# Kernel tuning notes

Measured on AMD Instinct MI355X. Metric: run time of the kernel, lower is better.

## Reference

```python
import jax, jax.numpy as jnp
import numpy as np

N = 50000   # nodes per type (d and t)
E = 500000  # edges per relation
D = 128     # in = out features
NEG_SLOPE = 0.2


def setup_inputs() -> dict:
    key = jax.random.key(0)
    ks = jax.random.split(key, 24)
    s = 1.0 / np.sqrt(D)
    inp = {
        'x_d': jax.random.normal(ks[0], (N, D), jnp.float32),
        'x_t': jax.random.normal(ks[1], (N, D), jnp.float32),
        'W_dd': jax.random.normal(ks[2], (D, D), jnp.float32) * s,
        'W_tt': jax.random.normal(ks[3], (D, D), jnp.float32) * s,
        'W_dt': jax.random.normal(ks[4], (D, D), jnp.float32) * s,
        'al_dd': jax.random.normal(ks[5], (D,), jnp.float32) * s,
        'ar_dd': jax.random.normal(ks[6], (D,), jnp.float32) * s,
        'al_tt': jax.random.normal(ks[7], (D,), jnp.float32) * s,
        'ar_tt': jax.random.normal(ks[8], (D,), jnp.float32) * s,
        'al_dt': jax.random.normal(ks[9], (D,), jnp.float32) * s,
        'ar_dt': jax.random.normal(ks[10], (D,), jnp.float32) * s,
        'b_dd': jnp.zeros((D,), jnp.float32),
        'b_tt': jnp.zeros((D,), jnp.float32),
        'b_dt': jnp.zeros((D,), jnp.float32),
        'src_dd': jax.random.randint(ks[11], (E,), 0, N),
        'dst_dd': jax.random.randint(ks[12], (E,), 0, N),
        'src_tt': jax.random.randint(ks[13], (E,), 0, N),
        'dst_tt': jax.random.randint(ks[14], (E,), 0, N),
        'src_dt': jax.random.randint(ks[15], (E,), 0, N),
        'dst_dt': jax.random.randint(ks[16], (E,), 0, N),
        'src_td': jax.random.randint(ks[17], (E,), 0, N),
        'dst_td': jax.random.randint(ks[18], (E,), 0, N),
    }
    return inp


def _gat(x_src, x_dst, W, al, ar, b, src, dst, n_dst):
    """DGL GATConv (num_heads=1, no dropout, eval): gather -> edge attn ->
    per-destination segment softmax -> scatter-weighted aggregation + bias."""
    fs = x_src @ W                      # [Ns, D]
    fd = x_dst @ W                      # [Nd, D]
    el = fs @ al                        # [Ns]
    er = fd @ ar                        # [Nd]
    e = jax.nn.leaky_relu(el[src] + er[dst], NEG_SLOPE)   # [E]
    m = jax.ops.segment_max(e, dst, num_segments=n_dst)
    m = jnp.where(jnp.isfinite(m), m, jnp.float32(0))      # isolated dst nodes
    ex = jnp.exp(e - m[dst])
    ssum = jax.ops.segment_sum(ex, dst, num_segments=n_dst)
    alpha = ex / ssum[dst]              # [E]
    out = jax.ops.segment_sum(alpha[:, None] * fs[src], dst, num_segments=n_dst)
    return out + b


def reference(x_d, x_t, W_dd, W_tt, W_dt,
              al_dd, ar_dd, al_tt, ar_tt, al_dt, ar_dt,
              b_dd, b_tt, b_dt,
              src_dd, dst_dd, src_tt, dst_tt,
              src_dt, dst_dt, src_td, dst_td):
    # HeteroGraphConv with aggregate='sum'; 'dt' and 'td' share parameters.
    h_d = (_gat(x_d, x_d, W_dd, al_dd, ar_dd, b_dd, src_dd, dst_dd, N)
           + _gat(x_t, x_d, W_dt, al_dt, ar_dt, b_dt, src_td, dst_td, N))
    h_t = (_gat(x_t, x_t, W_tt, al_tt, ar_tt, b_tt, src_tt, dst_tt, N)
           + _gat(x_d, x_t, W_dt, al_dt, ar_dt, b_dt, src_dt, dst_dt, N))
    return jnp.stack([h_d, h_t])        # [2, N, D]
```

## Files before the change

kernel.cpp:

```cpp
#include <hip/hip_runtime.h>
#include <hip/hip_bf16.h>
#include <hip/hip_fp16.h>
#include <math.h>

#define DD 128
#define NEG_SLOPE 0.2f
#define CAP_B 2048
#define BSHIFT 7
#define MAXNB 512
#define NSCAT 160

typedef __attribute__((ext_vector_type(8))) short bf16x8;
typedef __attribute__((ext_vector_type(4))) float f32x4;
typedef __attribute__((ext_vector_type(8))) unsigned short u16x8;

__device__ __forceinline__ short f2bf(float f) {
    __hip_bfloat16 h = __float2bfloat16(f);
    return __builtin_bit_cast(short, h);
}
__device__ __forceinline__ float bf2f(unsigned short u) {
    return __uint_as_float(((unsigned)u) << 16);
}
__device__ __forceinline__ unsigned short f2h(float f) {
    return __builtin_bit_cast(unsigned short, __float2half(f));
}
__device__ __forceinline__ float h2f(unsigned short u) {
    return __half2float(__builtin_bit_cast(__half, u));
}
__device__ __forceinline__ float lrexp(float e) {
    e = (e > 0.f) ? e : NEG_SLOPE * e;
    return __expf(e);
}

__device__ __forceinline__ int permcol(int cp) { return (cp & 7) * 16 + (cp >> 3); }

__global__ __launch_bounds__(256) void pack_init_k(
    const float* __restrict__ W0, const float* __restrict__ W1,
    const float* __restrict__ W2,
    unsigned short* __restrict__ P0, unsigned short* __restrict__ P1,
    unsigned short* __restrict__ P2, int* __restrict__ cursor,
    const float* __restrict__ b_dd, const float* __restrict__ b_tt,
    const float* __restrict__ b_dt, float* __restrict__ pb0,
    float* __restrict__ pb1)
{
    if (blockIdx.x >= 24) {
        const int i = (blockIdx.x - 24) * 256 + threadIdx.x;
        if (i < 4 * MAXNB) cursor[i] = (i & (MAXNB - 1)) * CAP_B;
        if (blockIdx.x == 24) {
            const int t = threadIdx.x;
            if (t < 128) pb0[t] = b_dd[permcol(t)] + b_dt[permcol(t)];
            else         pb1[t - 128] = b_tt[permcol(t - 128)] + b_dt[permcol(t - 128)];
        }
        return;
    }
    const int t = blockIdx.x * 256 + threadIdx.x;
    const int m = t >> 11;
    const int r = t & 2047;
    const float* W = (m == 0) ? W0 : (m == 1) ? W1 : W2;
    unsigned short* P = (m == 0) ? P0 : (m == 1) ? P1 : P2;
    const int lane = r & 63;
    const int tile = r >> 6;
    const int ks = tile >> 3, ct = tile & 7;
    const int col = ct * 16 + (lane & 15);
    const int k0 = ks * 32 + (lane >> 4) * 8;
#pragma unroll
    for (int j = 0; j < 8; ++j)
        P[(size_t)r * 8 + j] = (unsigned short)f2bf(W[(size_t)(k0 + j) * DD + col]);
}

__device__ __forceinline__ void epi_store(
    f32x4 acc[8], const float* __restrict__ al, const float* __restrict__ ar,
    unsigned short* __restrict__ fb, float* __restrict__ el,
    float* __restrict__ er, int r0, int lane, int nrows)
{
    float pl[4] = {0.f, 0.f, 0.f, 0.f};
    float pr[4] = {0.f, 0.f, 0.f, 0.f};
#pragma unroll
    for (int ct = 0; ct < 8; ++ct) {
        const float alc = al[ct * 16 + (lane & 15)];
        const float arc = ar[ct * 16 + (lane & 15)];
#pragma unroll
        for (int g = 0; g < 4; ++g) {
            pl[g] = fmaf(acc[ct][g], alc, pl[g]);
            pr[g] = fmaf(acc[ct][g], arc, pr[g]);
        }
    }
#pragma unroll
    for (int o = 1; o < 16; o <<= 1) {
#pragma unroll
        for (int g = 0; g < 4; ++g) {
            pl[g] += __shfl_xor(pl[g], o, 16);
            pr[g] += __shfl_xor(pr[g], o, 16);
        }
    }
    if ((lane & 15) == 0) {
#pragma unroll
        for (int g = 0; g < 4; ++g) {
            const int r = r0 + (lane >> 4) * 4 + g;
            if (r < nrows) { el[r] = pl[g]; er[r] = pr[g]; }
        }
    }
#pragma unroll
    for (int g = 0; g < 4; ++g) {
        const int r = r0 + (lane >> 4) * 4 + g;
        if (r < nrows) {
            u16x8 v;
#pragma unroll
            for (int ct = 0; ct < 8; ++ct)
                v[ct] = (unsigned short)f2bf(acc[ct][g]);
            *((u16x8*)(fb + (size_t)r * DD + (lane & 15) * 8)) = v;
        }
    }
}

struct Prep5Args {
    const float* x[4];
    const unsigned short* Wp[4];
    const float* al[4]; const float* ar[4];
    unsigned short* fb[4]; float* el[4]; float* er[4];
    const int* src[4]; const int* dst[4];
    int* cursor; unsigned* ebuf;
    int n, nE, nb;
};

__global__ __launch_bounds__(512) void prep5_k(Prep5Args P)
{
    __shared__ unsigned short wlds[2048 * 8];

    const int v = blockIdx.y;
    if (v < 4) {
        const int lane = threadIdx.x & 63;
        const int wave = threadIdx.x >> 6;
        const int r0 = (blockIdx.x * 8 + wave) * 16;
        if (blockIdx.x * 128 >= P.n) return;

        const uint4* wsrc = (const uint4*)P.Wp[v];
        uint4* wdst = (uint4*)wlds;
#pragma unroll
        for (int i = 0; i < 4; ++i)
            wdst[threadIdx.x + i * 512] = wsrc[threadIdx.x + i * 512];
        __syncthreads();

        if (r0 >= P.n) return;
        const int arow = r0 + (lane & 15);
        const int arow_c = (arow < P.n) ? arow : (P.n - 1);
        const int kbase = (lane >> 4) * 8;
        const float* x = P.x[v];

        f32x4 acc[8];
#pragma unroll
        for (int ct = 0; ct < 8; ++ct) acc[ct] = (f32x4)(0.f);

#pragma unroll
        for (int ks = 0; ks < 4; ++ks) {
            const float* xp = x + (size_t)arow_c * DD + ks * 32 + kbase;
            const float4 a0 = ((const float4*)xp)[0];
            const float4 a1 = ((const float4*)xp)[1];
            bf16x8 af;
            af[0] = f2bf(a0.x); af[1] = f2bf(a0.y); af[2] = f2bf(a0.z); af[3] = f2bf(a0.w);
            af[4] = f2bf(a1.x); af[5] = f2bf(a1.y); af[6] = f2bf(a1.z); af[7] = f2bf(a1.w);
#pragma unroll
            for (int ct = 0; ct < 8; ++ct) {
                const bf16x8 w = *((const bf16x8*)(wlds + ((size_t)(ks * 8 + ct) * 64 + lane) * 8));
                acc[ct] = __builtin_amdgcn_mfma_f32_16x16x32_bf16(af, w, acc[ct], 0, 0, 0);
            }
        }
        epi_store(acc, P.al[v], P.ar[v], P.fb[v], P.el[v], P.er[v], r0, lane, P.n);
        return;
    }

    const int sb = blockIdx.x;
    if (sb >= 4 * NSCAT) return;
    int* cnt_s  = (int*)wlds;
    int* base_s = ((int*)wlds) + MAXNB;
    const int rel = sb / NSCAT;
    const int blk = sb - rel * NSCAT;
    const int* src = P.src[rel];
    const int* dst = P.dst[rel];
    int* cur = P.cursor + (size_t)rel * MAXNB;
    unsigned* eb = P.ebuf + (size_t)rel * P.nb * CAP_B;

    const int t = threadIdx.x;
    const int ch = (P.nE + NSCAT - 1) / NSCAT;
    const int i0 = blk * ch;
    const int i1 = (i0 + ch < P.nE) ? (i0 + ch) : P.nE;

    for (int i = t; i < MAXNB; i += 512) cnt_s[i] = 0;
    __syncthreads();
    for (int i = i0 + t; i < i1; i += 512)
        atomicAdd(&cnt_s[dst[i] >> BSHIFT], 1);
    __syncthreads();
    for (int b = t; b < P.nb; b += 512) {
        const int c = cnt_s[b];
        base_s[b] = c ? atomicAdd(cur + b, c) : 0;
        cnt_s[b] = 0;
    }
    __syncthreads();
    for (int i = i0 + t; i < i1; i += 512) {
        const int dv = dst[i];
        const int b = dv >> BSHIFT;
        const int p = base_s[b] + atomicAdd(&cnt_s[b], 1);
        eb[p] = ((unsigned)(dv & ((1 << BSHIFT) - 1)) << 16) | (unsigned)src[i];
    }
}

struct SortArgs {
    const float* el[4]; const float* er[4];
};

__global__ __launch_bounds__(256) void sort_alpha_k(
    const unsigned* __restrict__ ebuf, const int* __restrict__ cursor,
    SortArgs S, unsigned* __restrict__ cs32, int* __restrict__ rstart,
    int* __restrict__ rdeg, int n, int nb)
{
    const int b = blockIdx.x, rel = blockIdx.y, t = threadIdx.x;
    int cnt = cursor[(size_t)rel * MAXNB + b] - b * CAP_B;
    cnt = (cnt < 0) ? 0 : (cnt > CAP_B) ? CAP_B : cnt;

    __shared__ unsigned buf[CAP_B];
    __shared__ unsigned out32[CAP_B];
    __shared__ int hist[128], off[128], cnt2[128], excl[128];
    __shared__ float ssum[128];
    __shared__ int total_s;

    const unsigned* ebr = ebuf + ((size_t)rel * nb + b) * CAP_B;
    for (int i = t; i < cnt; i += 256) buf[i] = ebr[i];
    if (t < 128) { hist[t] = 0; cnt2[t] = 0; ssum[t] = 0.f; }
    __syncthreads();
    for (int i = t; i < cnt; i += 256) atomicAdd(&hist[buf[i] >> 16], 1);
    __syncthreads();
    if (t < 128) off[t] = (hist[t] + 3) & ~3;
    __syncthreads();
    for (int o = 1; o < 128; o <<= 1) {
        const int v = (t < 128 && t >= o) ? off[t - o] : 0;
        __syncthreads();
        if (t < 128) off[t] += v;
        __syncthreads();
    }
    if (t < 128) {
        const int pc = (hist[t] + 3) & ~3;
        excl[t] = off[t] - pc;
        const int d = b * 128 + t;
        if (d < n) {
            rstart[(size_t)rel * n + d] = b * CAP_B + excl[t];
            rdeg[(size_t)rel * n + d] = pc;
        }
        for (int i = excl[t] + hist[t]; i < off[t]; ++i) out32[i] = 0u;
    }
    if (t == 127) total_s = off[127];
    __syncthreads();

    const float* el = S.el[rel];
    const float* er = S.er[rel];
    for (int i = t; i < cnt; i += 256) {
        const unsigned v = buf[i];
        const int local = v >> 16;
        const int s = v & 0xffffu;
        const float ex = lrexp(el[s] + er[b * 128 + local]);
        atomicAdd(&ssum[local], ex);
        const int p = excl[local] + atomicAdd(&cnt2[local], 1);
        out32[p] = (unsigned)s | ((unsigned)f2h(ex) << 16);
    }
    __syncthreads();
    if (t < 128 && hist[t] > 0) {
        const float inv = 1.f / ssum[t];
        const int e0 = excl[t], e1 = excl[t] + hist[t];
        for (int i = e0; i < e1; ++i) {
            const unsigned v = out32[i];
            const float alpha = h2f((unsigned short)(v >> 16)) * inv;
            out32[i] = (v & 0xffffu) | ((unsigned)f2h(alpha) << 16);
        }
    }
    __syncthreads();
    unsigned* cs = cs32 + ((size_t)rel * nb + b) * CAP_B;
    const int total = total_s;
    for (int i = t; i < total; i += 256) cs[i] = out32[i];
}

struct AggArgs {
    const int* rs[4]; const int* rd[4];
    const unsigned* cs[4];
    const unsigned short* fb[4];
    const float* pb[2];
    float* out[2];
    int n;
};

__device__ __forceinline__ void fma8(
    float a, const u16x8& v, float4& o0, float4& o1)
{
    o0.x = fmaf(a, bf2f(v[0]), o0.x);
    o0.y = fmaf(a, bf2f(v[1]), o0.y);
    o0.z = fmaf(a, bf2f(v[2]), o0.z);
    o0.w = fmaf(a, bf2f(v[3]), o0.w);
    o1.x = fmaf(a, bf2f(v[4]), o1.x);
    o1.y = fmaf(a, bf2f(v[5]), o1.y);
    o1.z = fmaf(a, bf2f(v[6]), o1.z);
    o1.w = fmaf(a, bf2f(v[7]), o1.w);
}

__device__ __forceinline__ void agg16p(
    const int* __restrict__ rs, const int* __restrict__ rd,
    const unsigned* __restrict__ cs, const unsigned short* __restrict__ fb,
    int d, int lane, float4& o0, float4& o1)
{
    const int cnt = rd[d];
    if (cnt == 0) return;
    const unsigned* csp = cs + rs[d];
    int k = 0;
    for (; k + 8 <= cnt; k += 8) {
        unsigned pv[8];
#pragma unroll
        for (int j = 0; j < 8; ++j) pv[j] = csp[k + j];
        u16x8 v[8];
#pragma unroll
        for (int j = 0; j < 8; ++j)
            v[j] = ((const u16x8*)(fb + (size_t)(pv[j] & 0xffffu) * DD))[lane];
#pragma unroll
        for (int j = 0; j < 8; ++j)
            fma8(h2f((unsigned short)(pv[j] >> 16)), v[j], o0, o1);
    }
    for (; k + 4 <= cnt; k += 4) {
        unsigned pv[4];
#pragma unroll
        for (int j = 0; j < 4; ++j) pv[j] = csp[k + j];
        u16x8 v[4];
#pragma unroll
        for (int j = 0; j < 4; ++j)
            v[j] = ((const u16x8*)(fb + (size_t)(pv[j] & 0xffffu) * DD))[lane];
#pragma unroll
        for (int j = 0; j < 4; ++j)
            fma8(h2f((unsigned short)(pv[j] >> 16)), v[j], o0, o1);
    }
}

__global__ __launch_bounds__(256) void gat_aggregate_f(AggArgs A)
{
    const int lane = threadIdx.x & 15;
    const int grp  = threadIdx.x >> 4;
    const int gid = blockIdx.x * 16 + grp;
    if (gid >= 2 * A.n) return;
    const int ty = (gid >= A.n) ? 1 : 0;
    const int d = gid - ty * A.n;
    const int sl1 = ty ? 1 : 0;
    const int sl2 = ty ? 2 : 3;

    float4 o0 = ((const float4*)A.pb[ty])[lane * 2];
    float4 o1 = ((const float4*)A.pb[ty])[lane * 2 + 1];

    agg16p(A.rs[sl1], A.rd[sl1], A.cs[sl1], A.fb[sl1], d, lane, o0, o1);
    agg16p(A.rs[sl2], A.rd[sl2], A.cs[sl2], A.fb[sl2], d, lane, o0, o1);

    float* op = A.out[ty] + (size_t)d * DD + lane;
    op[0]   = o0.x; op[16]  = o0.y; op[32]  = o0.z; op[48]  = o0.w;
    op[64]  = o1.x; op[80]  = o1.y; op[96]  = o1.z; op[112] = o1.w;
}

extern "C" void kernel_launch(void* const* d_in, const int* in_sizes, int n_in,
                              void* d_out, int out_size, void* d_ws, size_t ws_size,
                              hipStream_t stream)
{
    const float* x_d  = (const float*)d_in[0];
    const float* x_t  = (const float*)d_in[1];
    const float* W_dd = (const float*)d_in[2];
    const float* W_tt = (const float*)d_in[3];
    const float* W_dt = (const float*)d_in[4];
    const float* al_dd = (const float*)d_in[5];
    const float* ar_dd = (const float*)d_in[6];
    const float* al_tt = (const float*)d_in[7];
    const float* ar_tt = (const float*)d_in[8];
    const float* al_dt = (const float*)d_in[9];
    const float* ar_dt = (const float*)d_in[10];
    const float* b_dd  = (const float*)d_in[11];
    const float* b_tt  = (const float*)d_in[12];
    const float* b_dt  = (const float*)d_in[13];
    const int* src_dd = (const int*)d_in[14];
    const int* dst_dd = (const int*)d_in[15];
    const int* src_tt = (const int*)d_in[16];
    const int* dst_tt = (const int*)d_in[17];
    const int* src_dt = (const int*)d_in[18];
    const int* dst_dt = (const int*)d_in[19];
    const int* src_td = (const int*)d_in[20];
    const int* dst_td = (const int*)d_in[21];

    const int n  = in_sizes[0] / DD;
    const int nE = in_sizes[14];
    const int nb = (n + 127) >> BSHIFT;

    float* ws = (float*)d_ws;
    size_t off = 0;
    unsigned short* fb_dd   = (unsigned short*)(ws + off); off += (size_t)n * DD / 2;
    unsigned short* fb_tt   = (unsigned short*)(ws + off); off += (size_t)n * DD / 2;
    unsigned short* fb_dt_d = (unsigned short*)(ws + off); off += (size_t)n * DD / 2;
    unsigned short* fb_dt_t = (unsigned short*)(ws + off); off += (size_t)n * DD / 2;
    unsigned* ebuf = (unsigned*)(ws + off); off += (size_t)4 * nb * CAP_B;
    unsigned* cs32 = (unsigned*)(ws + off); off += (size_t)4 * nb * CAP_B;
    float* el_dd   = ws + off; off += n;
    float* er_dd   = ws + off; off += n;
    float* el_tt   = ws + off; off += n;
    float* er_tt   = ws + off; off += n;
    float* el_dt_d = ws + off; off += n;
    float* er_dt_d = ws + off; off += n;
    float* el_dt_t = ws + off; off += n;
    float* er_dt_t = ws + off; off += n;
    int* rstart = (int*)(ws + off); off += (size_t)4 * n;
    int* rdeg   = (int*)(ws + off); off += (size_t)4 * n;
    int* cursor = (int*)(ws + off); off += (size_t)4 * MAXNB;
    unsigned short* Wp_dd = (unsigned short*)(ws + off); off += 2048 * 8 / 2;
    unsigned short* Wp_tt = (unsigned short*)(ws + off); off += 2048 * 8 / 2;
    unsigned short* Wp_dt = (unsigned short*)(ws + off); off += 2048 * 8 / 2;
    float* pb0 = ws + off; off += DD;
    float* pb1 = ws + off; off += DD;

    if (ws_size < off * sizeof(float)) return;

    pack_init_k<<<32, 256, 0, stream>>>(W_dd, W_tt, W_dt, Wp_dd, Wp_tt, Wp_dt,
                                        cursor, b_dd, b_tt, b_dt, pb0, pb1);

    Prep5Args P;
    P.x[0] = x_d; P.x[1] = x_t; P.x[2] = x_d; P.x[3] = x_t;
    P.Wp[0] = Wp_dd; P.Wp[1] = Wp_tt; P.Wp[2] = Wp_dt; P.Wp[3] = Wp_dt;
    P.al[0] = al_dd; P.al[1] = al_tt; P.al[2] = al_dt; P.al[3] = al_dt;
    P.ar[0] = ar_dd; P.ar[1] = ar_tt; P.ar[2] = ar_dt; P.ar[3] = ar_dt;
    P.fb[0] = fb_dd; P.fb[1] = fb_tt; P.fb[2] = fb_dt_d; P.fb[3] = fb_dt_t;
    P.el[0] = el_dd; P.el[1] = el_tt; P.el[2] = el_dt_d; P.el[3] = el_dt_t;
    P.er[0] = er_dd; P.er[1] = er_tt; P.er[2] = er_dt_d; P.er[3] = er_dt_t;
    P.src[0] = src_dd; P.dst[0] = dst_dd;
    P.src[1] = src_tt; P.dst[1] = dst_tt;
    P.src[2] = src_dt; P.dst[2] = dst_dt;
    P.src[3] = src_td; P.dst[3] = dst_td;
    P.cursor = cursor; P.ebuf = ebuf;
    P.n = n; P.nE = nE; P.nb = nb;

    int gx = (n + 127) / 128;
    if (gx < 4 * NSCAT) gx = 4 * NSCAT;
    dim3 pgrid(gx, 5);
    prep5_k<<<pgrid, 512, 0, stream>>>(P);

    SortArgs S;
    S.el[0] = el_dd;   S.er[0] = er_dd;
    S.el[1] = el_tt;   S.er[1] = er_tt;
    S.el[2] = el_dt_d; S.er[2] = er_dt_t;
    S.el[3] = el_dt_t; S.er[3] = er_dt_d;
    dim3 bgrid(nb, 4);
    sort_alpha_k<<<bgrid, 256, 0, stream>>>(ebuf, cursor, S, cs32, rstart, rdeg, n, nb);

    const size_t reg = (size_t)nb * CAP_B;
    AggArgs A;
    A.rs[0] = rstart + 0 * (size_t)n; A.rd[0] = rdeg + 0 * (size_t)n;
    A.rs[1] = rstart + 1 * (size_t)n; A.rd[1] = rdeg + 1 * (size_t)n;
    A.rs[2] = rstart + 2 * (size_t)n; A.rd[2] = rdeg + 2 * (size_t)n;
    A.rs[3] = rstart + 3 * (size_t)n; A.rd[3] = rdeg + 3 * (size_t)n;
    A.cs[0] = cs32 + 0 * reg; A.cs[1] = cs32 + 1 * reg;
    A.cs[2] = cs32 + 2 * reg; A.cs[3] = cs32 + 3 * reg;
    A.fb[0] = fb_dd; A.fb[1] = fb_tt;
    A.fb[2] = fb_dt_d;
    A.fb[3] = fb_dt_t;
    A.pb[0] = pb0; A.pb[1] = pb1;
    A.out[0] = (float*)d_out;
    A.out[1] = (float*)d_out + (size_t)n * DD;
    A.n = n;

    const int aggrid = (2 * n + 15) / 16;
    gat_aggregate_f<<<aggrid, 256, 0, stream>>>(A);
}
```

Baseline: 145.1 us.

## Use persistent tiled GEMM blocks and per-block multi-relation scatter in prep kernel

The prep kernel now launches a fixed grid of 160 blocks per relation. Each GEMM block loads the packed weight into LDS once and loops over row tiles with a stride, instead of one block per 128-row tile that reloads W every time. The scatter blocks each handle their edge chunk for all four relations in sequence, instead of one block per relation-chunk. This cuts the block count and redundant weight loads, but lowers parallelism for the scatter phase and adds serial work per block.

```diff
diff --git a/kernel.cpp b/kernel.cpp
--- a/kernel.cpp
+++ b/kernel.cpp
@@ -9,6 +9,7 @@
 #define BSHIFT 7
 #define MAXNB 512
 #define NSCAT 160
+#define TBLK 160
 
 typedef __attribute__((ext_vector_type(8))) short bf16x8;
 typedef __attribute__((ext_vector_type(4))) float f32x4;
@@ -113,94 +114,96 @@
     }
 }
 
-struct Prep5Args {
+struct Prep6Args {
     const float* x[4];
     const unsigned short* Wp[4];
     const float* al[4]; const float* ar[4];
     unsigned short* fb[4]; float* el[4]; float* er[4];
     const int* src[4]; const int* dst[4];
     int* cursor; unsigned* ebuf;
-    int n, nE, nb;
+    int n, nE, nb, ntiles;
 };
 
-__global__ __launch_bounds__(512) void prep5_k(Prep5Args P)
+__global__ __launch_bounds__(512) void prep6_k(Prep6Args P)
 {
     __shared__ unsigned short wlds[2048 * 8];
 
     const int v = blockIdx.y;
     if (v < 4) {
+        const uint4* wsrc = (const uint4*)P.Wp[v];
+        uint4* wdst = (uint4*)wlds;
+#pragma unroll
+        for (int i = 0; i < 4; ++i)
+            wdst[threadIdx.x + i * 512] = wsrc[threadIdx.x + i * 512];
+        __syncthreads();
+
         const int lane = threadIdx.x & 63;
         const int wave = threadIdx.x >> 6;
-        const int r0 = (blockIdx.x * 8 + wave) * 16;
-        if (blockIdx.x * 128 >= P.n) return;
-
-        const uint4* wsrc = (const uint4*)P.Wp[v];
-        uint4* wdst = (uint4*)wlds;
-#pragma unroll
-        for (int i = 0; i < 4; ++i)
-            wdst[threadIdx.x + i * 512] = wsrc[threadIdx.x + i * 512];
-        __syncthreads();
-
-        if (r0 >= P.n) return;
-        const int arow = r0 + (lane & 15);
-        const int arow_c = (arow < P.n) ? arow : (P.n - 1);
         const int kbase = (lane >> 4) * 8;
         const float* x = P.x[v];
 
-        f32x4 acc[8];
-#pragma unroll
-        for (int ct = 0; ct < 8; ++ct) acc[ct] = (f32x4)(0.f);
-
-#pragma unroll
-        for (int ks = 0; ks < 4; ++ks) {
-            const float* xp = x + (size_t)arow_c * DD + ks * 32 + kbase;
-            const float4 a0 = ((const float4*)xp)[0];
-            const float4 a1 = ((const float4*)xp)[1];
-            bf16x8 af;
-            af[0] = f2bf(a0.x); af[1] = f2bf(a0.y); af[2] = f2bf(a0.z); af[3] = f2bf(a0.w);
-            af[4] = f2bf(a1.x); af[5] = f2bf(a1.y); af[6] = f2bf(a1.z); af[7] = f2bf(a1.w);
-#pragma unroll
-            for (int ct = 0; ct < 8; ++ct) {
-                const bf16x8 w = *((const bf16x8*)(wlds + ((size_t)(ks * 8 + ct) * 64 + lane) * 8));
-                acc[ct] = __builtin_amdgcn_mfma_f32_16x16x32_bf16(af, w, acc[ct], 0, 0, 0);
+        for (int tile = blockIdx.x; tile < P.ntiles; tile += TBLK) {
+            const int r0 = (tile * 8 + wave) * 16;
+            if (r0 >= P.n) continue;
+            const int arow = r0 + (lane & 15);
+            const int arow_c = (arow < P.n) ? arow : (P.n - 1);
+
+            f32x4 acc[8];
+#pragma unroll
+            for (int ct = 0; ct < 8; ++ct) acc[ct] = (f32x4)(0.f);
+
+#pragma unroll
+            for (int ks = 0; ks < 4; ++ks) {
+                const float* xp = x + (size_t)arow_c * DD + ks * 32 + kbase;
+                const float4 a0 = ((const float4*)xp)[0];
+                const float4 a1 = ((const float4*)xp)[1];
+                bf16x8 af;
+                af[0] = f2bf(a0.x); af[1] = f2bf(a0.y); af[2] = f2bf(a0.z); af[3] = f2bf(a0.w);
+                af[4] = f2bf(a1.x); af[5] = f2bf(a1.y); af[6] = f2bf(a1.z); af[7] = f2bf(a1.w);
+#pragma unroll
+                for (int ct = 0; ct < 8; ++ct) {
+                    const bf16x8 w = *((const bf16x8*)(wlds + ((size_t)(ks * 8 + ct) * 64 + lane) * 8));
+                    acc[ct] = __builtin_amdgcn_mfma_f32_16x16x32_bf16(af, w, acc[ct], 0, 0, 0);
+                }
             }
-        }
-        epi_store(acc, P.al[v], P.ar[v], P.fb[v], P.el[v], P.er[v], r0, lane, P.n);
+            epi_store(acc, P.al[v], P.ar[v], P.fb[v], P.el[v], P.er[v], r0, lane, P.n);
+        }
         return;
     }
 
     const int sb = blockIdx.x;
-    if (sb >= 4 * NSCAT) return;
+    if (sb >= NSCAT) return;
     int* cnt_s  = (int*)wlds;
     int* base_s = ((int*)wlds) + MAXNB;
-    const int rel = sb / NSCAT;
-    const int blk = sb - rel * NSCAT;
-    const int* src = P.src[rel];
-    const int* dst = P.dst[rel];
-    int* cur = P.cursor + (size_t)rel * MAXNB;
-    unsigned* eb = P.ebuf + (size_t)rel * P.nb * CAP_B;
-
     const int t = threadIdx.x;
     const int ch = (P.nE + NSCAT - 1) / NSCAT;
-    const int i0 = blk * ch;
+    const int i0 = sb * ch;
     const int i1 = (i0 + ch < P.nE) ? (i0 + ch) : P.nE;
 
-    for (int i = t; i < MAXNB; i += 512) cnt_s[i] = 0;
-    __syncthreads();
-    for (int i = i0 + t; i < i1; i += 512)
-        atomicAdd(&cnt_s[dst[i] >> BSHIFT], 1);
-    __syncthreads();
-    for (int b = t; b < P.nb; b += 512) {
-        const int c = cnt_s[b];
-        base_s[b] = c ? atomicAdd(cur + b, c) : 0;
-        cnt_s[b] = 0;
-    }
-    __syncthreads();
-    for (int i = i0 + t; i < i1; i += 512) {
-        const int dv = dst[i];
-        const int b = dv >> BSHIFT;
-        const int p = base_s[b] + atomicAdd(&cnt_s[b], 1);
-        eb[p] = ((unsigned)(dv & ((1 << BSHIFT) - 1)) << 16) | (unsigned)src[i];
+    for (int rel = 0; rel < 4; ++rel) {
+        const int* src = P.src[rel];
+        const int* dst = P.dst[rel];
+        int* cur = P.cursor + (size_t)rel * MAXNB;
+        unsigned* eb = P.ebuf + (size_t)rel * P.nb * CAP_B;
+
+        for (int i = t; i < MAXNB; i += 512) cnt_s[i] = 0;
+        __syncthreads();
+        for (int i = i0 + t; i < i1; i += 512)
+            atomicAdd(&cnt_s[dst[i] >> BSHIFT], 1);
+        __syncthreads();
+        for (int b = t; b < P.nb; b += 512) {
+            const int c = cnt_s[b];
+            base_s[b] = c ? atomicAdd(cur + b, c) : 0;
+            cnt_s[b] = 0;
+        }
+        __syncthreads();
+        for (int i = i0 + t; i < i1; i += 512) {
+            const int dv = dst[i];
+            const int b = dv >> BSHIFT;
+            const int p = base_s[b] + atomicAdd(&cnt_s[b], 1);
+            eb[p] = ((unsigned)(dv & ((1 << BSHIFT) - 1)) << 16) | (unsigned)src[i];
+        }
+        __syncthreads();
     }
 }
 
@@ -286,7 +289,7 @@
     int n;
 };
 
-__device__ __forceinline__ void fma8(
+__device__ __forceinline__ void fma8v(
     float a, const u16x8& v, float4& o0, float4& o1)
 {
     o0.x = fmaf(a, bf2f(v[0]), o0.x);
@@ -318,7 +321,7 @@
             v[j] = ((const u16x8*)(fb + (size_t)(pv[j] & 0xffffu) * DD))[lane];
 #pragma unroll
         for (int j = 0; j < 8; ++j)
-            fma8(h2f((unsigned short)(pv[j] >> 16)), v[j], o0, o1);
+            fma8v(h2f((unsigned short)(pv[j] >> 16)), v[j], o0, o1);
     }
     for (; k + 4 <= cnt; k += 4) {
         unsigned pv[4];
@@ -330,7 +333,7 @@
             v[j] = ((const u16x8*)(fb + (size_t)(pv[j] & 0xffffu) * DD))[lane];
 #pragma unroll
         for (int j = 0; j < 4; ++j)
-            fma8(h2f((unsigned short)(pv[j] >> 16)), v[j], o0, o1);
+            fma8v(h2f((unsigned short)(pv[j] >> 16)), v[j], o0, o1);
     }
 }
 
@@ -386,6 +389,7 @@
     const int n  = in_sizes[0] / DD;
     const int nE = in_sizes[14];
     const int nb = (n + 127) >> BSHIFT;
+    const int ntiles = (n + 127) / 128;
 
     float* ws = (float*)d_ws;
     size_t off = 0;
@@ -417,7 +421,7 @@
     pack_init_k<<<32, 256, 0, stream>>>(W_dd, W_tt, W_dt, Wp_dd, Wp_tt, Wp_dt,
                                         cursor, b_dd, b_tt, b_dt, pb0, pb1);
 
-    Prep5Args P;
+    Prep6Args P;
     P.x[0] = x_d; P.x[1] = x_t; P.x[2] = x_d; P.x[3] = x_t;
     P.Wp[0] = Wp_dd; P.Wp[1] = Wp_tt; P.Wp[2] = Wp_dt; P.Wp[3] = Wp_dt;
     P.al[0] = al_dd; P.al[1] = al_tt; P.al[2] = al_dt; P.al[3] = al_dt;
@@ -430,12 +434,10 @@
     P.src[2] = src_dt; P.dst[2] = dst_dt;
     P.src[3] = src_td; P.dst[3] = dst_td;
     P.cursor = cursor; P.ebuf = ebuf;
-    P.n = n; P.nE = nE; P.nb = nb;
-
-    int gx = (n + 127) / 128;
-    if (gx < 4 * NSCAT) gx = 4 * NSCAT;
-    dim3 pgrid(gx, 5);
-    prep5_k<<<pgrid, 512, 0, stream>>>(P);
+    P.n = n; P.nE = nE; P.nb = nb; P.ntiles = ntiles;
+
+    dim3 pgrid(TBLK, 5);
+    prep6_k<<<pgrid, 512, 0, stream>>>(P);
 
     SortArgs S;
     S.el[0] = el_dd;   S.er[0] = er_dd;
```

New measurement: 154.6 us. 6.5% more time.

## Merge both relations per destination type into one CSR with flag bit

Applied to the files above, without the earlier changes.

The sort kernel now handles both relations that feed a destination type in one block. It builds a single combined per-destination edge list in which the high bit marks which relation and feature table each edge uses, and keeps separate softmax sums per relation. The aggregate kernel then walks one list per destination instead of two, which cuts per-node padding to multiples of four and halves the loop overheads and rstart/rdeg loads. In exchange, each block uses twice the shared memory, which may reduce occupancy, only half as many sort blocks are launched, and the gather adds a per-edge select between feature tables.

```diff
diff --git a/kernel.cpp b/kernel.cpp
--- a/kernel.cpp
+++ b/kernel.cpp
@@ -204,30 +204,38 @@
     }
 }
 
-struct SortArgs {
-    const float* el[4]; const float* er[4];
+struct Sort2Args {
+    const float* elA[2]; const float* erA[2];
+    const float* elB[2]; const float* erB[2];
 };
 
-__global__ __launch_bounds__(256) void sort_alpha_k(
+__global__ __launch_bounds__(256) void sort_alpha2_k(
     const unsigned* __restrict__ ebuf, const int* __restrict__ cursor,
-    SortArgs S, unsigned* __restrict__ cs32, int* __restrict__ rstart,
+    Sort2Args S, unsigned* __restrict__ cs32, int* __restrict__ rstart,
     int* __restrict__ rdeg, int n, int nb)
 {
-    const int b = blockIdx.x, rel = blockIdx.y, t = threadIdx.x;
-    int cnt = cursor[(size_t)rel * MAXNB + b] - b * CAP_B;
-    cnt = (cnt < 0) ? 0 : (cnt > CAP_B) ? CAP_B : cnt;
-
-    __shared__ unsigned buf[CAP_B];
-    __shared__ unsigned out32[CAP_B];
+    const int b = blockIdx.x, ty = blockIdx.y, t = threadIdx.x;
+    const int relA = ty;
+    const int relB = ty ? 2 : 3;
+    int cntA = cursor[(size_t)relA * MAXNB + b] - b * CAP_B;
+    cntA = (cntA < 0) ? 0 : (cntA > CAP_B) ? CAP_B : cntA;
+    int cntB = cursor[(size_t)relB * MAXNB + b] - b * CAP_B;
+    cntB = (cntB < 0) ? 0 : (cntB > CAP_B) ? CAP_B : cntB;
+    const int cnt = cntA + cntB;
+
+    __shared__ unsigned buf[2 * CAP_B];
+    __shared__ unsigned out32[2 * CAP_B];
     __shared__ int hist[128], off[128], cnt2[128], excl[128];
-    __shared__ float ssum[128];
+    __shared__ float ssumA[128], ssumB[128];
     __shared__ int total_s;
 
-    const unsigned* ebr = ebuf + ((size_t)rel * nb + b) * CAP_B;
-    for (int i = t; i < cnt; i += 256) buf[i] = ebr[i];
-    if (t < 128) { hist[t] = 0; cnt2[t] = 0; ssum[t] = 0.f; }
-    __syncthreads();
-    for (int i = t; i < cnt; i += 256) atomicAdd(&hist[buf[i] >> 16], 1);
+    const unsigned* ebA = ebuf + ((size_t)relA * nb + b) * CAP_B;
+    const unsigned* ebB = ebuf + ((size_t)relB * nb + b) * CAP_B;
+    for (int i = t; i < cntA; i += 256) buf[i] = ebA[i];
+    for (int i = t; i < cntB; i += 256) buf[cntA + i] = ebB[i] | 0x80000000u;
+    if (t < 128) { hist[t] = 0; cnt2[t] = 0; ssumA[t] = 0.f; ssumB[t] = 0.f; }
+    __syncthreads();
+    for (int i = t; i < cnt; i += 256) atomicAdd(&hist[(buf[i] >> 16) & 0x7f], 1);
     __syncthreads();
     if (t < 128) off[t] = (hist[t] + 3) & ~3;
     __syncthreads();
@@ -242,51 +250,58 @@
         excl[t] = off[t] - pc;
         const int d = b * 128 + t;
         if (d < n) {
-            rstart[(size_t)rel * n + d] = b * CAP_B + excl[t];
-            rdeg[(size_t)rel * n + d] = pc;
+            rstart[(size_t)ty * n + d] = b * (2 * CAP_B) + excl[t];
+            rdeg[(size_t)ty * n + d] = pc;
         }
         for (int i = excl[t] + hist[t]; i < off[t]; ++i) out32[i] = 0u;
     }
     if (t == 127) total_s = off[127];
     __syncthreads();
 
-    const float* el = S.el[rel];
-    const float* er = S.er[rel];
+    const float* elA = S.elA[ty]; const float* erA = S.erA[ty];
+    const float* elB = S.elB[ty]; const float* erB = S.erB[ty];
     for (int i = t; i < cnt; i += 256) {
         const unsigned v = buf[i];
-        const int local = v >> 16;
+        const unsigned flag = v >> 31;
+        const int local = (v >> 16) & 0x7f;
         const int s = v & 0xffffu;
-        const float ex = lrexp(el[s] + er[b * 128 + local]);
-        atomicAdd(&ssum[local], ex);
+        const int d = b * 128 + local;
+        const float e = flag ? (elB[s] + erB[d]) : (elA[s] + erA[d]);
+        const float ex = lrexp(e);
+        atomicAdd(flag ? &ssumB[local] : &ssumA[local], ex);
         const int p = excl[local] + atomicAdd(&cnt2[local], 1);
-        out32[p] = (unsigned)s | ((unsigned)f2h(ex) << 16);
+        out32[p] = (unsigned)s | ((unsigned)f2h(ex) << 16) | (flag << 31);
     }
     __syncthreads();
     if (t < 128 && hist[t] > 0) {
-        const float inv = 1.f / ssum[t];
+        const float invA = (ssumA[t] > 0.f) ? 1.f / ssumA[t] : 0.f;
+        const float invB = (ssumB[t] > 0.f) ? 1.f / ssumB[t] : 0.f;
         const int e0 = excl[t], e1 = excl[t] + hist[t];
         for (int i = e0; i < e1; ++i) {
             const unsigned v = out32[i];
-            const float alpha = h2f((unsigned short)(v >> 16)) * inv;
-            out32[i] = (v & 0xffffu) | ((unsigned)f2h(alpha) << 16);
-        }
-    }
-    __syncthreads();
-    unsigned* cs = cs32 + ((size_t)rel * nb + b) * CAP_B;
+            const unsigned flag = v >> 31;
+            const float a = h2f((unsigned short)((v >> 16) & 0x7fff)) *
+                            (flag ? invB : invA);
+            out32[i] = (v & 0xffffu) | ((unsigned)f2h(a) << 16) | (flag << 31);
+        }
+    }
+    __syncthreads();
+    unsigned* cs = cs32 + ((size_t)ty * nb + b) * (2 * CAP_B);
     const int total = total_s;
     for (int i = t; i < total; i += 256) cs[i] = out32[i];
 }
 
 struct AggArgs {
-    const int* rs[4]; const int* rd[4];
-    const unsigned* cs[4];
-    const unsigned short* fb[4];
+    const int* rs; const int* rd;
+    const unsigned* cs[2];
+    const unsigned short* fbA[2];
+    const unsigned short* fbB[2];
     const float* pb[2];
     float* out[2];
     int n;
 };
 
-__device__ __forceinline__ void fma8(
+__device__ __forceinline__ void fma8v(
     float a, const u16x8& v, float4& o0, float4& o1)
 {
     o0.x = fmaf(a, bf2f(v[0]), o0.x);
@@ -299,41 +314,6 @@
     o1.w = fmaf(a, bf2f(v[7]), o1.w);
 }
 
-__device__ __forceinline__ void agg16p(
-    const int* __restrict__ rs, const int* __restrict__ rd,
-    const unsigned* __restrict__ cs, const unsigned short* __restrict__ fb,
-    int d, int lane, float4& o0, float4& o1)
-{
-    const int cnt = rd[d];
-    if (cnt == 0) return;
-    const unsigned* csp = cs + rs[d];
-    int k = 0;
-    for (; k + 8 <= cnt; k += 8) {
-        unsigned pv[8];
-#pragma unroll
-        for (int j = 0; j < 8; ++j) pv[j] = csp[k + j];
-        u16x8 v[8];
-#pragma unroll
-        for (int j = 0; j < 8; ++j)
-            v[j] = ((const u16x8*)(fb + (size_t)(pv[j] & 0xffffu) * DD))[lane];
-#pragma unroll
-        for (int j = 0; j < 8; ++j)
-            fma8(h2f((unsigned short)(pv[j] >> 16)), v[j], o0, o1);
-    }
-    for (; k + 4 <= cnt; k += 4) {
-        unsigned pv[4];
-#pragma unroll
-        for (int j = 0; j < 4; ++j) pv[j] = csp[k + j];
-        u16x8 v[4];
-#pragma unroll
-        for (int j = 0; j < 4; ++j)
-            v[j] = ((const u16x8*)(fb + (size_t)(pv[j] & 0xffffu) * DD))[lane];
-#pragma unroll
-        for (int j = 0; j < 4; ++j)
-            fma8(h2f((unsigned short)(pv[j] >> 16)), v[j], o0, o1);
-    }
-}
-
 __global__ __launch_bounds__(256) void gat_aggregate_f(AggArgs A)
 {
     const int lane = threadIdx.x & 15;
@@ -342,14 +322,45 @@
     if (gid >= 2 * A.n) return;
     const int ty = (gid >= A.n) ? 1 : 0;
     const int d = gid - ty * A.n;
-    const int sl1 = ty ? 1 : 0;
-    const int sl2 = ty ? 2 : 3;
 
     float4 o0 = ((const float4*)A.pb[ty])[lane * 2];
     float4 o1 = ((const float4*)A.pb[ty])[lane * 2 + 1];
 
-    agg16p(A.rs[sl1], A.rd[sl1], A.cs[sl1], A.fb[sl1], d, lane, o0, o1);
-    agg16p(A.rs[sl2], A.rd[sl2], A.cs[sl2], A.fb[sl2], d, lane, o0, o1);
+    const unsigned short* fbA = A.fbA[ty];
+    const unsigned short* fbB = A.fbB[ty];
+    const int cnt = A.rd[(size_t)ty * A.n + d];
+    if (cnt > 0) {
+        const unsigned* csp = A.cs[ty] + A.rs[(size_t)ty * A.n + d];
+        int k = 0;
+        for (; k + 8 <= cnt; k += 8) {
+            unsigned pv[8];
+#pragma unroll
+            for (int j = 0; j < 8; ++j) pv[j] = csp[k + j];
+            u16x8 v[8];
+#pragma unroll
+            for (int j = 0; j < 8; ++j) {
+                const unsigned short* fb = (pv[j] >> 31) ? fbB : fbA;
+                v[j] = ((const u16x8*)(fb + (size_t)(pv[j] & 0xffffu) * DD))[lane];
+            }
+#pragma unroll
+            for (int j = 0; j < 8; ++j)
+                fma8v(h2f((unsigned short)((pv[j] >> 16) & 0x7fff)), v[j], o0, o1);
+        }
+        for (; k + 4 <= cnt; k += 4) {
+            unsigned pv[4];
+#pragma unroll
+            for (int j = 0; j < 4; ++j) pv[j] = csp[k + j];
+            u16x8 v[4];
+#pragma unroll
+            for (int j = 0; j < 4; ++j) {
+                const unsigned short* fb = (pv[j] >> 31) ? fbB : fbA;
+                v[j] = ((const u16x8*)(fb + (size_t)(pv[j] & 0xffffu) * DD))[lane];
+            }
+#pragma unroll
+            for (int j = 0; j < 4; ++j)
+                fma8v(h2f((unsigned short)((pv[j] >> 16) & 0x7fff)), v[j], o0, o1);
+        }
+    }
 
     float* op = A.out[ty] + (size_t)d * DD + lane;
     op[0]   = o0.x; op[16]  = o0.y; op[32]  = o0.z; op[48]  = o0.w;
@@ -394,7 +405,7 @@
     unsigned short* fb_dt_d = (unsigned short*)(ws + off); off += (size_t)n * DD / 2;
     unsigned short* fb_dt_t = (unsigned short*)(ws + off); off += (size_t)n * DD / 2;
     unsigned* ebuf = (unsigned*)(ws + off); off += (size_t)4 * nb * CAP_B;
-    unsigned* cs32 = (unsigned*)(ws + off); off += (size_t)4 * nb * CAP_B;
+    unsigned* cs32 = (unsigned*)(ws + off); off += (size_t)2 * nb * (2 * CAP_B);
     float* el_dd   = ws + off; off += n;
     float* er_dd   = ws + off; off += n;
     float* el_tt   = ws + off; off += n;
@@ -403,8 +414,8 @@
     float* er_dt_d = ws + off; off += n;
     float* el_dt_t = ws + off; off += n;
     float* er_dt_t = ws + off; off += n;
-    int* rstart = (int*)(ws + off); off += (size_t)4 * n;
-    int* rdeg   = (int*)(ws + off); off += (size_t)4 * n;
+    int* rstart = (int*)(ws + off); off += (size_t)2 * n;
+    int* rdeg   = (int*)(ws + off); off += (size_t)2 * n;
     int* cursor = (int*)(ws + off); off += (size_t)4 * MAXNB;
     unsigned short* Wp_dd = (unsigned short*)(ws + off); off += 2048 * 8 / 2;
     unsigned short* Wp_tt = (unsigned short*)(ws + off); off += 2048 * 8 / 2;
@@ -437,25 +448,20 @@
     dim3 pgrid(gx, 5);
     prep5_k<<<pgrid, 512, 0, stream>>>(P);
 
-    SortArgs S;
-    S.el[0] = el_dd;   S.er[0] = er_dd;
-    S.el[1] = el_tt;   S.er[1] = er_tt;
-    S.el[2] = el_dt_d; S.er[2] = er_dt_t;
-    S.el[3] = el_dt_t; S.er[3] = er_dt_d;
-    dim3 bgrid(nb, 4);
-    sort_alpha_k<<<bgrid, 256, 0, stream>>>(ebuf, cursor, S, cs32, rstart, rdeg, n, nb);
-
-    const size_t reg = (size_t)nb * CAP_B;
+    Sort2Args S;
+    S.elA[0] = el_dd;   S.erA[0] = er_dd;
+    S.elA[1] = el_tt;   S.erA[1] = er_tt;
+    S.elB[0] = el_dt_t; S.erB[0] = er_dt_d;
+    S.elB[1] = el_dt_d; S.erB[1] = er_dt_t;
+    dim3 bgrid(nb, 2);
+    sort_alpha2_k<<<bgrid, 256, 0, stream>>>(ebuf, cursor, S, cs32, rstart, rdeg, n, nb);
+
     AggArgs A;
-    A.rs[0] = rstart + 0 * (size_t)n; A.rd[0] = rdeg + 0 * (size_t)n;
-    A.rs[1] = rstart + 1 * (size_t)n; A.rd[1] = rdeg + 1 * (size_t)n;
-    A.rs[2] = rstart + 2 * (size_t)n; A.rd[2] = rdeg + 2 * (size_t)n;
-    A.rs[3] = rstart + 3 * (size_t)n; A.rd[3] = rdeg + 3 * (size_t)n;
-    A.cs[0] = cs32 + 0 * reg; A.cs[1] = cs32 + 1 * reg;
-    A.cs[2] = cs32 + 2 * reg; A.cs[3] = cs32 + 3 * reg;
-    A.fb[0] = fb_dd; A.fb[1] = fb_tt;
-    A.fb[2] = fb_dt_d;
-    A.fb[3] = fb_dt_t;
+    A.rs = rstart; A.rd = rdeg;
+    A.cs[0] = cs32;
+    A.cs[1] = cs32 + (size_t)nb * (2 * CAP_B);
+    A.fbA[0] = fb_dd;   A.fbA[1] = fb_tt;
+    A.fbB[0] = fb_dt_t; A.fbB[1] = fb_dt_d;
     A.pb[0] = pb0; A.pb[1] = pb1;
     A.out[0] = (float*)d_out;
     A.out[1] = (float*)d_out + (size_t)n * DD;
```

Result: slower. 151.6 us (+4.5%).
